# Performance work log

Hardware: AMD Instinct MI355X
Metric: run time of the kernel (lower is better)

The kernel has to match this reference:

```python
import jax, jax.numpy as jnp
import numpy as np

B, L, D_MODEL = 2, 2048, 1024
D_STATE, D_CONV, EXPAND, DT_RANK = 16, 4, 2, 64
D_INNER = EXPAND * D_MODEL


def setup_inputs() -> dict:
    key = jax.random.key(0)
    ks = jax.random.split(key, 12)
    s = 0.02
    A_log = jnp.log(jnp.broadcast_to(jnp.arange(1, D_STATE + 1, dtype=jnp.float32), (D_INNER, D_STATE)))
    return {
        "x": jax.random.normal(ks[0], (B, L, D_MODEL), jnp.float32),
        "W_in": jax.random.normal(ks[1], (2 * D_INNER, D_MODEL), jnp.float32) * s,
        "conv_w": jax.random.normal(ks[2], (D_INNER, 1, D_CONV), jnp.float32) * 0.2,
        "conv_b": jax.random.normal(ks[3], (D_INNER,), jnp.float32) * s,
        "W_xp": jax.random.normal(ks[4], (DT_RANK + 2 * D_STATE, D_INNER), jnp.float32) * s,
        "W_dt": jax.random.normal(ks[5], (D_INNER, DT_RANK), jnp.float32) * 0.1,
        "b_dt": jax.random.uniform(ks[6], (D_INNER,), jnp.float32, -4.6, -2.3),  # ~softplus^-1 of small dt
        "A_log": A_log,
        "D": jnp.ones((D_INNER,), jnp.float32),
        "W_out_ssm": jax.random.normal(ks[7], (D_MODEL, D_INNER), jnp.float32) * s,
        "W_out": jax.random.normal(ks[8], (D_MODEL, D_MODEL), jnp.float32) * s,
        "b_out": jnp.zeros((D_MODEL,), jnp.float32),
    }


def _mamba_block(x, W_in, conv_w, conv_b, W_xp, W_dt, b_dt, A_log, D, W_out_ssm, W_out, b_out):
    d_inner = conv_b.shape[0]
    d_state = A_log.shape[1]
    dt_rank = W_dt.shape[1]
    d_conv = conv_w.shape[-1]

    # in_proj -> x branch and gate z
    xz = x @ W_in.T                         # [B, L, 2*d_inner]
    xin, z = jnp.split(xz, 2, axis=-1)

    # causal depthwise conv over time
    xc = jnp.transpose(xin, (0, 2, 1))      # [B, d_inner, L]
    xc = jax.lax.conv_general_dilated(
        xc, conv_w, window_strides=(1,), padding=[(d_conv - 1, 0)],
        feature_group_count=d_inner)
    xc = jax.nn.silu(xc + conv_b[None, :, None])
    xs = jnp.transpose(xc, (0, 2, 1))       # [B, L, d_inner]

    # input-dependent dt, B, C
    x_dbl = xs @ W_xp.T                     # [B, L, dt_rank + 2*d_state]
    dt, Bm, Cm = jnp.split(x_dbl, [dt_rank, dt_rank + d_state], axis=-1)
    dt = jax.nn.softplus(dt @ W_dt.T + b_dt)  # [B, L, d_inner]

    A = -jnp.exp(A_log)                     # [d_inner, d_state]

    def step(h, inp):
        dt_t, B_t, C_t, x_t = inp           # [B,di] [B,ds] [B,ds] [B,di]
        dA = jnp.exp(dt_t[:, :, None] * A)                      # [B, di, ds]
        h = h * dA + (dt_t * x_t)[:, :, None] * B_t[:, None, :]  # [B, di, ds]
        y = jnp.einsum('bds,bs->bd', h, C_t)
        return h, y

    h0 = jnp.zeros((x.shape[0], d_inner, d_state), x.dtype)
    tm = lambda a: jnp.swapaxes(a, 0, 1)    # time-major
    _, ys = jax.lax.scan(step, h0, (tm(dt), tm(Bm), tm(Cm), tm(xs)))
    y = jnp.swapaxes(ys, 0, 1)              # [B, L, d_inner]

    y = y + xs * D
    y = y * jax.nn.silu(z)
    y = y @ W_out_ssm.T                     # mamba-internal out_proj -> d_model
    return y @ W_out.T + b_out              # wrapper out_proj


def reference(x, W_in, conv_w, conv_b, W_xp, W_dt, b_dt, A_log, D, W_out_ssm, W_out, b_out):
    return _mamba_block(x, W_in, conv_w, conv_b, W_xp, W_dt, b_dt, A_log, D, W_out_ssm, W_out, b_out)
```

## Files before the change

kernel.cpp:

```cpp
#include <hip/hip_runtime.h>
#include <hip/hip_bf16.h>
#include <cmath>
#include <cstdint>

typedef __bf16 bf16_t;
typedef bf16_t bf16x8 __attribute__((ext_vector_type(8)));
typedef bf16_t bf16x4 __attribute__((ext_vector_type(4)));
typedef float f32x4 __attribute__((ext_vector_type(4)));

#define BB 2
#define LL 2048
#define DMODEL 1024
#define DINNER 2048
#define DSTATE 16
#define NC 64
#define CHUNK 32
#define KSEG 256

#define EXP2F(x) __builtin_amdgcn_exp2f(x)

#define CVT_N0 1048576
#define CVT_N1 2097152
#define CVT_N2 2129920
#define CVT_N3 2392064
#define CVT_NB0 9344
#define CVT_NB1 10368
#define CVT_NBT 10880
__global__ __launch_bounds__(256) void k_cvt_all(
    const float* __restrict__ x, const float* __restrict__ Win,
    const float* __restrict__ Wdt, const float* __restrict__ Wo,
    const float* __restrict__ Wxp, const float* __restrict__ Wos,
    bf16_t* __restrict__ x_b, bf16_t* __restrict__ Win_b,
    bf16_t* __restrict__ Wdt_b, bf16_t* __restrict__ Wo_b,
    bf16_t* __restrict__ Wxp_b, bf16_t* __restrict__ WosT_b) {
    const int tid = threadIdx.x;
    if (blockIdx.x < CVT_NB0) {
        int i = blockIdx.x * 256 + tid;
        const float* src; bf16_t* dst; int j;
        if (i < CVT_N0)      { src = x;   dst = x_b;   j = i; }
        else if (i < CVT_N1) { src = Win; dst = Win_b; j = i - CVT_N0; }
        else if (i < CVT_N2) { src = Wdt; dst = Wdt_b; j = i - CVT_N1; }
        else                 { src = Wo;  dst = Wo_b;  j = i - CVT_N2; }
        float4 v = reinterpret_cast<const float4*>(src)[j];
        bf16x4 o;
        o[0] = (bf16_t)v.x; o[1] = (bf16_t)v.y; o[2] = (bf16_t)v.z; o[3] = (bf16_t)v.w;
        reinterpret_cast<bf16x4*>(dst)[j] = o;
    } else if (blockIdx.x < CVT_NB1) {
        int i = (blockIdx.x - CVT_NB0) * 256 + tid;
        int r = i >> 11, c = i & (DINNER - 1);
        float v = (r < 96) ? Wxp[r * DINNER + c] : 0.f;
        Wxp_b[i] = (bf16_t)v;
    } else {
        __shared__ float tile[64][65];
        const int bid = blockIdx.x - CVT_NB1;
        const int m0 = (bid & 15) * 64;
        const int d0 = (bid >> 4) * 64;
        const int dl = tid & 63;
        #pragma unroll 4
        for (int i = 0; i < 16; ++i) {
            const int mr = (tid >> 6) + i * 4;
            tile[dl][mr] = Wos[(size_t)(m0 + mr) * DINNER + d0 + dl];
        }
        __syncthreads();
        const int dr = tid >> 2;
        const int q  = tid & 3;
        bf16_t* op = WosT_b + (size_t)(d0 + dr) * DMODEL + m0 + q * 16;
        bf16x8 v0, v1;
        #pragma unroll
        for (int j = 0; j < 8; ++j) v0[j] = (bf16_t)tile[dr][q * 16 + j];
        #pragma unroll
        for (int j = 0; j < 8; ++j) v1[j] = (bf16_t)tile[dr][q * 16 + 8 + j];
        reinterpret_cast<bf16x8*>(op)[0] = v0;
        reinterpret_cast<bf16x8*>(op)[1] = v1;
    }
}

__device__ __forceinline__ void gload16(const void* g, void* l) {
    __builtin_amdgcn_global_load_lds(
        (const __attribute__((address_space(1))) void*)g,
        (__attribute__((address_space(3))) void*)l,
        16, 0, 0);
}

__global__ __launch_bounds__(512) void k_gemm256(
    const bf16_t* __restrict__ x_b, const bf16_t* __restrict__ Win_b,
    bf16_t* __restrict__ xin_b, bf16_t* __restrict__ zsT) {
    __shared__ bf16_t lds[65536];
    const int tid = threadIdx.x;
    const int wid = tid >> 6, lane = tid & 63;

    const int bid = (blockIdx.x & 7) * 32 + (blockIdx.x >> 3);
    const bf16_t* A; const bf16_t* Bt; int m0, n0, sub;
    if (bid < 128) {
        sub = 0; A = x_b; Bt = Win_b;
        m0 = (bid >> 3) * 256; n0 = (bid & 7) * 256;
    } else {
        sub = 1; A = Win_b + (size_t)DINNER * DMODEL; Bt = x_b;
        const int t2 = bid - 128;
        m0 = (t2 >> 4) * 256; n0 = (t2 & 15) * 256;
    }
    const int wr = wid >> 2, wc = wid & 3;
    f32x4 acc[8][4] = {};

    const int srow = tid >> 3;
    const int k8p = (tid & 7) ^ (srow & 7);
    const bf16_t* apA = A + (size_t)(m0 + srow) * 1024 + k8p * 8;
    const bf16_t* apB = Bt + (size_t)(n0 + srow) * 1024 + k8p * 8;

    auto stageA = [&](int slot, int kt) {
        char* b0 = (char*)lds + slot * 32768 + wid * 1024;
        const bf16_t* src = apA + kt * 64;
        gload16(src, b0);
        gload16(src + (size_t)64 * 1024, b0 + 8192);
        gload16(src + (size_t)128 * 1024, b0 + 16384);
        gload16(src + (size_t)192 * 1024, b0 + 24576);
    };
    auto stageB = [&](int slot, int kt) {
        char* b0 = (char*)lds + 65536 + slot * 32768 + wid * 1024;
        const bf16_t* src = apB + kt * 64;
        gload16(src, b0);
        gload16(src + (size_t)64 * 1024, b0 + 8192);
        gload16(src + (size_t)128 * 1024, b0 + 16384);
        gload16(src + (size_t)192 * 1024, b0 + 24576);
    };

    const int lm = lane & 15, lq = lane >> 4;

    const bf16_t* pA0[8]; const bf16_t* pA1[8];
    const bf16_t* pB0[4]; const bf16_t* pB1[4];
    #pragma unroll
    for (int i = 0; i < 8; ++i) {
        const int rr = lm + i * 16;
        const int e0 = wr * 8192 + rr * 64 + (lq ^ (rr & 7)) * 8;
        pA0[i] = lds + e0;
        pA1[i] = lds + (e0 ^ 32);
    }
    #pragma unroll
    for (int j = 0; j < 4; ++j) {
        const int rr = (wc & 1) * 64 + lm + j * 16;
        const int e0 = 32768 + (wc >> 1) * 8192 + rr * 64 + (lq ^ (rr & 7)) * 8;
        pB0[j] = lds + e0;
        pB1[j] = lds + (e0 ^ 32);
    }

    auto body = [&](int t, int s) {
        asm volatile("s_waitcnt vmcnt(0)" ::: "memory");
        __builtin_amdgcn_sched_barrier(0);
        __builtin_amdgcn_s_barrier();
        __builtin_amdgcn_sched_barrier(0);
        if (t + 1 < 16) {
            stageA(s ^ 1, t + 1);
            stageB(s ^ 1, t + 1);
        }
        {
            bf16x8 fa[8], fb[4];
            #pragma unroll
            for (int i = 0; i < 8; ++i) fa[i] = *(const bf16x8*)(pA0[i] + s * 16384);
            #pragma unroll
            for (int j = 0; j < 4; ++j) fb[j] = *(const bf16x8*)(pB0[j] + s * 16384);
            __builtin_amdgcn_s_setprio(1);
            #pragma unroll
            for (int i = 0; i < 8; ++i)
                #pragma unroll
                for (int j = 0; j < 4; ++j)
                    acc[i][j] = __builtin_amdgcn_mfma_f32_16x16x32_bf16(fa[i], fb[j], acc[i][j], 0, 0, 0);
            __builtin_amdgcn_s_setprio(0);
        }
        {
            bf16x8 fa[8], fb[4];
            #pragma unroll
            for (int i = 0; i < 8; ++i) fa[i] = *(const bf16x8*)(pA1[i] + s * 16384);
            #pragma unroll
            for (int j = 0; j < 4; ++j) fb[j] = *(const bf16x8*)(pB1[j] + s * 16384);
            __builtin_amdgcn_s_setprio(1);
            #pragma unroll
            for (int i = 0; i < 8; ++i)
                #pragma unroll
                for (int j = 0; j < 4; ++j)
                    acc[i][j] = __builtin_amdgcn_mfma_f32_16x16x32_bf16(fa[i], fb[j], acc[i][j], 0, 0, 0);
            __builtin_amdgcn_s_setprio(0);
        }
    };

    stageA(0, 0);
    stageB(0, 0);
    for (int tt = 0; tt < 8; ++tt) {
        body(2 * tt, 0);
        body(2 * tt + 1, 1);
    }

    const int row0 = m0 + wr * 128 + lq * 4;
    const int col0 = n0 + wc * 64 + lm;
    #pragma unroll
    for (int i = 0; i < 8; ++i) {
        #pragma unroll
        for (int j = 0; j < 4; ++j) {
            #pragma unroll
            for (int r = 0; r < 4; ++r) {
                const int row = row0 + i * 16 + r;
                const int c = col0 + j * 16;
                float v = acc[i][j][r];
                if (sub == 0) xin_b[(size_t)row * DINNER + c] = (bf16_t)v;
                else          zsT[(size_t)row * (BB * LL) + c] = (bf16_t)(v / (1.f + __expf(-v)));
            }
        }
    }
}

enum { EPI_BF16 = 0, EPI_BIAS = 1, EPI_SOFTPLUS_RB = 3, EPI_PARTK = 4 };

template <int EPI>
__global__ __launch_bounds__(512) void k_gemm_cd128(
    const bf16_t* __restrict__ A, const bf16_t* __restrict__ Bt,
    int N, int Ktiles, int lda, int ldb,
    float* __restrict__ C, bf16_t* __restrict__ Cb,
    const float* __restrict__ bias) {
    __shared__ bf16_t lds[32768];
    const int tid = threadIdx.x;
    const int wid = tid >> 6, lane = tid & 63;
    const int bx = (blockIdx.x & 7) * ((int)gridDim.x >> 3) + (blockIdx.x >> 3);
    const int ntile = N >> 7;
    const int m0 = (bx / ntile) << 7;
    const int n0 = (bx % ntile) << 7;
    const int wr = wid >> 2, wc = wid & 3;
    f32x4 acc[4][2] = {};

    const int srow = tid >> 3;
    const int k8p = (tid & 7) ^ (srow & 7);
    const bf16_t* apA = A + (size_t)(m0 + srow) * lda + k8p * 8;
    const bf16_t* apB = Bt + (size_t)(n0 + srow) * ldb + k8p * 8;

    auto stageA = [&](int slot, int kt) {
        char* b0 = (char*)lds + slot * 16384 + wid * 1024;
        const bf16_t* src = apA + kt * 64;
        gload16(src, b0);
        gload16(src + (size_t)64 * lda, b0 + 8192);
    };
    auto stageB = [&](int slot, int kt) {
        char* b0 = (char*)lds + 32768 + slot * 16384 + wid * 1024;
        const bf16_t* src = apB + kt * 64;
        gload16(src, b0);
        gload16(src + (size_t)64 * ldb, b0 + 8192);
    };

    const int lm = lane & 15, lq = lane >> 4;

    const bf16_t* pA0[4]; const bf16_t* pA1[4];
    const bf16_t* pB0[2]; const bf16_t* pB1[2];
    #pragma unroll
    for (int i = 0; i < 4; ++i) {
        const int rr = lm + i * 16;
        const int e0 = wr * 4096 + rr * 64 + (lq ^ (rr & 7)) * 8;
        pA0[i] = lds + e0;
        pA1[i] = lds + (e0 ^ 32);
    }
    #pragma unroll
    for (int j = 0; j < 2; ++j) {
        const int rr = wc * 32 + lm + j * 16;
        const int e0 = 16384 + rr * 64 + (lq ^ (rr & 7)) * 8;
        pB0[j] = lds + e0;
        pB1[j] = lds + (e0 ^ 32);
    }

    auto body = [&](int t, int s) {
        asm volatile("s_waitcnt vmcnt(0)" ::: "memory");
        __builtin_amdgcn_sched_barrier(0);
        __builtin_amdgcn_s_barrier();
        __builtin_amdgcn_sched_barrier(0);
        if (t + 1 < Ktiles) {
            stageA(s ^ 1, t + 1);
            stageB(s ^ 1, t + 1);
        }
        {
            bf16x8 fa[4], fb[2];
            #pragma unroll
            for (int i = 0; i < 4; ++i) fa[i] = *(const bf16x8*)(pA0[i] + s * 8192);
            #pragma unroll
            for (int j = 0; j < 2; ++j) fb[j] = *(const bf16x8*)(pB0[j] + s * 8192);
            __builtin_amdgcn_s_setprio(1);
            #pragma unroll
            for (int i = 0; i < 4; ++i)
                #pragma unroll
                for (int j = 0; j < 2; ++j)
                    acc[i][j] = __builtin_amdgcn_mfma_f32_16x16x32_bf16(fa[i], fb[j], acc[i][j], 0, 0, 0);
            __builtin_amdgcn_s_setprio(0);
        }
        {
            bf16x8 fa[4], fb[2];
            #pragma unroll
            for (int i = 0; i < 4; ++i) fa[i] = *(const bf16x8*)(pA1[i] + s * 8192);
            #pragma unroll
            for (int j = 0; j < 2; ++j) fb[j] = *(const bf16x8*)(pB1[j] + s * 8192);
            __builtin_amdgcn_s_setprio(1);
            #pragma unroll
            for (int i = 0; i < 4; ++i)
                #pragma unroll
                for (int j = 0; j < 2; ++j)
                    acc[i][j] = __builtin_amdgcn_mfma_f32_16x16x32_bf16(fa[i], fb[j], acc[i][j], 0, 0, 0);
            __builtin_amdgcn_s_setprio(0);
        }
    };

    stageA(0, 0);
    stageB(0, 0);
    for (int tt = 0; tt < (Ktiles >> 1); ++tt) {
        body(2 * tt, 0);
        body(2 * tt + 1, 1);
    }

    const int row0 = m0 + wr * 64 + lq * 4;
    const int col0 = n0 + wc * 32 + lm;
    #pragma unroll
    for (int i = 0; i < 4; ++i) {
        #pragma unroll
        for (int j = 0; j < 2; ++j) {
            #pragma unroll
            for (int r = 0; r < 4; ++r) {
                const int row = row0 + i * 16 + r;
                const int c = col0 + j * 16;
                float v = acc[i][j][r];
                if (EPI == EPI_BF16) Cb[(size_t)row * N + c] = (bf16_t)v;
                else                 C[(size_t)row * N + c] = v + bias[c];
            }
        }
    }
}

template <int EPI>
__global__ __launch_bounds__(512) void k_gemm_bt(
    const bf16_t* __restrict__ A, const bf16_t* __restrict__ Bt,
    int M, int N, int Kloop, int lda, int ldb,
    float* __restrict__ C, bf16_t* __restrict__ Cb,
    const float* __restrict__ bias,
    float* __restrict__ o_part) {
    __shared__ bf16_t sA[2][128 * 32];
    __shared__ bf16_t sB[2][128 * 32];
    const int tid = threadIdx.x;
    const int wid = tid >> 6, lane = tid & 63;
    const int bx = (blockIdx.x & 7) * ((int)gridDim.x >> 3) + (blockIdx.x >> 3);
    int m0, n0, k0 = 0, seg = 0;
    if (EPI == EPI_PARTK) {
        m0 = (bx & 31) << 7;
        n0 = 0;
        seg = bx >> 5;
        k0 = seg * KSEG;
    } else {
        const int ntile = N >> 7;
        m0 = (bx / ntile) << 7;
        n0 = (bx % ntile) << 7;
    }
    const int wr = wid >> 2, wc = wid & 3;
    f32x4 acc[4][2] = {};

    const bf16_t* ap = A + (size_t)(m0 + (tid >> 2)) * lda + (tid & 3) * 8 + k0;
    const bf16_t* bp = Bt + (size_t)(n0 + (tid >> 2)) * ldb + (tid & 3) * 8 + k0;
    const int lm = lane & 15, lk = (lane >> 4) * 8;

    auto stage = [&](int buf, int kt) {
        char* dA = (char*)sA[buf] + wid * 1024;
        char* dB = (char*)sB[buf] + wid * 1024;
        gload16(ap + kt, dA);
        gload16(bp + kt, dB);
    };

    stage(0, 0);
    __syncthreads();
    int cur = 0;
    for (int kt = 0; kt < Kloop; kt += 32) {
        if (kt + 32 < Kloop) stage(cur ^ 1, kt + 32);
        const bf16_t* rA = sA[cur] + (wr * 64 + lm) * 32 + lk;
        const bf16_t* rB = sB[cur] + (wc * 32 + lm) * 32 + lk;
        bf16x8 fa[4], fb[2];
        #pragma unroll
        for (int i = 0; i < 4; ++i) fa[i] = *(const bf16x8*)(rA + i * 16 * 32);
        #pragma unroll
        for (int j = 0; j < 2; ++j) fb[j] = *(const bf16x8*)(rB + j * 16 * 32);
        __builtin_amdgcn_s_setprio(1);
        #pragma unroll
        for (int i = 0; i < 4; ++i)
            #pragma unroll
            for (int j = 0; j < 2; ++j)
                acc[i][j] = __builtin_amdgcn_mfma_f32_16x16x32_bf16(fa[i], fb[j], acc[i][j], 0, 0, 0);
        __builtin_amdgcn_s_setprio(0);
        __syncthreads();
        cur ^= 1;
    }

    const int row0 = m0 + wr * 64 + (lane >> 4) * 4;
    const int col0 = n0 + wc * 32 + lm;
    float* Cp = (EPI == EPI_PARTK)
        ? o_part + (size_t)seg * ((size_t)4096 * 128)
        : C;
    #pragma unroll
    for (int i = 0; i < 4; ++i) {
        #pragma unroll
        for (int j = 0; j < 2; ++j) {
            #pragma unroll
            for (int r = 0; r < 4; ++r) {
                int row = row0 + i * 16 + r;
                int c = col0 + j * 16;
                float v = acc[i][j][r];
                if (EPI == EPI_SOFTPLUS_RB) {
                    float xv = v + bias[row];
                    float sp = fmaxf(xv, 0.f) + log1pf(__expf(-fabsf(xv)));
                    Cb[(size_t)row * N + c] = (bf16_t)sp;
                } else {
                    Cp[(size_t)row * 128 + c] = v;
                }
            }
        }
    }
}

__global__ __launch_bounds__(256) void k_split_reduce(
    const float* __restrict__ part, bf16_t* __restrict__ dtr,
    float* __restrict__ Bmf, float* __restrict__ Cmf) {
    int idx = blockIdx.x * 256 + threadIdx.x;
    int row = idx >> 7, c = idx & 127;
    float s = 0.f;
    #pragma unroll
    for (int g = 0; g < 8; ++g) s += part[(size_t)g * (4096 * 128) + idx];
    if (c < 64) dtr[(size_t)row * 64 + c] = (bf16_t)s;
    else if (c < 80) Bmf[(size_t)row * 16 + (c - 64)] = s;
    else if (c < 96) Cmf[(size_t)row * 16 + (c - 80)] = s;
}

__global__ __launch_bounds__(256) void k_conv(
    const bf16_t* __restrict__ xin, const float* __restrict__ cw,
    const float* __restrict__ cb, bf16_t* __restrict__ xs_b,
    bf16_t* __restrict__ xsT) {
    __shared__ float tile[64][65];
    const int tid = threadIdx.x;
    const int d0  = (blockIdx.x & 31) * 64;
    const int bl0 = (blockIdx.x >> 5) * 64;
    const int dl = tid & 63;
    const int d  = d0 + dl;
    const float w0 = cw[d * 4], w1 = cw[d * 4 + 1], w2 = cw[d * 4 + 2], w3 = cw[d * 4 + 3];
    const float bias = cb[d];
    const int l0 = bl0 & (LL - 1);
    #pragma unroll 4
    for (int i = 0; i < 16; ++i) {
        const int blr = (tid >> 6) + i * 4;
        const int bl = bl0 + blr;
        const int l  = l0 + blr;
        const bf16_t* rp = xin + (size_t)bl * DINNER + d;
        float acc = fmaf(w3, (float)rp[0], bias);
        if (l >= 1) acc = fmaf(w2, (float)rp[-(int)DINNER], acc);
        if (l >= 2) acc = fmaf(w1, (float)rp[-2 * (int)DINNER], acc);
        if (l >= 3) acc = fmaf(w0, (float)rp[-3 * (int)DINNER], acc);
        float sv = acc / (1.f + __expf(-acc));
        xs_b[(size_t)bl * DINNER + d] = (bf16_t)sv;
        tile[dl][blr] = sv;
    }
    __syncthreads();
    const int dr = tid >> 2;
    const int q  = tid & 3;
    bf16_t* op = xsT + (size_t)(d0 + dr) * (BB * LL) + bl0 + q * 16;
    bf16x8 v0, v1;
    #pragma unroll
    for (int j = 0; j < 8; ++j) v0[j] = (bf16_t)tile[dr][q * 16 + j];
    #pragma unroll
    for (int j = 0; j < 8; ++j) v1[j] = (bf16_t)tile[dr][q * 16 + 8 + j];
    reinterpret_cast<bf16x8*>(op)[0] = v0;
    reinterpret_cast<bf16x8*>(op)[1] = v1;
}


__global__ __launch_bounds__(256) void k_scan_p1(
    const bf16_t* __restrict__ dtT, const bf16_t* __restrict__ xsT,
    const float* __restrict__ Bm, const float* __restrict__ A_log,
    bf16_t* __restrict__ alpha, bf16_t* __restrict__ beta) {
    __shared__ float sB[CHUNK * 16];
    const int db = blockIdx.x & 7;
    const int ck = (blockIdx.x >> 3) & (NC - 1);
    const int b  = blockIdx.x >> 9;
    const int tid = threadIdx.x;
    const int d  = db * 256 + tid;
    const int t0 = ck * CHUNK;

    const float* Bsrc = Bm + ((size_t)b * LL + t0) * 16;
    sB[tid] = Bsrc[tid];
    sB[tid + 256] = Bsrc[tid + 256];

    f32x4 a2[4];
    #pragma unroll
    for (int q = 0; q < 4; ++q) {
        f32x4 av = reinterpret_cast<const f32x4*>(A_log + d * 16)[q];
        #pragma unroll
        for (int j = 0; j < 4; ++j) a2[q][j] = -__expf(av[j]) * 1.44269504f;
    }
    const bf16x8* dtp = reinterpret_cast<const bf16x8*>(dtT + (size_t)d * (BB * LL) + b * LL + t0);
    const bf16x8* xsp = reinterpret_cast<const bf16x8*>(xsT + (size_t)d * (BB * LL) + b * LL + t0);

    bf16x8 dtl[4], xsl[4];
    #pragma unroll
    for (int q = 0; q < 4; ++q) dtl[q] = dtp[q];
    #pragma unroll
    for (int q = 0; q < 4; ++q) xsl[q] = xsp[q];

    __syncthreads();

    float al[16], be[16];
    #pragma unroll
    for (int s = 0; s < 16; ++s) { al[s] = 1.f; be[s] = 0.f; }

    #pragma unroll
    for (int t = 0; t < CHUNK; ++t) {
        float dtv = (float)dtl[t >> 3][t & 7];
        float xv  = (float)xsl[t >> 3][t & 7];
        float dtx = dtv * xv;
        #pragma unroll
        for (int q = 0; q < 4; ++q) {
            f32x4 Bq = *reinterpret_cast<const f32x4*>(sB + t * 16 + q * 4);
            #pragma unroll
            for (int j = 0; j < 4; ++j) {
                const int s = q * 4 + j;
                float dA = EXP2F(dtv * a2[q][j]);
                al[s] *= dA;
                be[s] = fmaf(be[s], dA, dtx * Bq[j]);
            }
        }
    }
    bf16_t* ap = alpha + ((size_t)(b * NC + ck)) * (DINNER * 16) + (size_t)d * 16;
    bf16_t* bp = beta  + ((size_t)(b * NC + ck)) * (DINNER * 16) + (size_t)d * 16;
    bf16x8 av0, av1, bv0, bv1;
    #pragma unroll
    for (int j = 0; j < 8; ++j) {
        av0[j] = (bf16_t)al[j];     av1[j] = (bf16_t)al[8 + j];
        bv0[j] = (bf16_t)be[j];     bv1[j] = (bf16_t)be[8 + j];
    }
    reinterpret_cast<bf16x8*>(ap)[0] = av0;
    reinterpret_cast<bf16x8*>(ap)[1] = av1;
    reinterpret_cast<bf16x8*>(bp)[0] = bv0;
    reinterpret_cast<bf16x8*>(bp)[1] = bv1;
}

__global__ __launch_bounds__(256) void k_scan_p2(
    const bf16_t* __restrict__ alpha, const bf16_t* __restrict__ beta,
    bf16_t* __restrict__ H) {
    const int gid = blockIdx.x * 256 + threadIdx.x;
    const int b = gid >> 15, r = gid & 32767;
    float h = 0.f;
    #pragma unroll 8
    for (int ck = 0; ck < NC; ++ck) {
        const size_t i = ((size_t)(b * NC + ck)) * 32768 + r;
        H[i] = (bf16_t)h;
        h = fmaf((float)alpha[i], h, (float)beta[i]);
    }
}

__global__ __launch_bounds__(256) void k_scan_p3(
    const bf16_t* __restrict__ dtT, const bf16_t* __restrict__ xsT,
    const float* __restrict__ Bm, const float* __restrict__ Cm,
    const bf16_t* __restrict__ zsT, const float* __restrict__ A_log,
    const float* __restrict__ Dp, const bf16_t* __restrict__ H,
    bf16_t* __restrict__ y) {
    __shared__ float sB[CHUNK * 16];
    __shared__ float sC[CHUNK * 16];
    const int db = blockIdx.x & 7;
    const int ck = (blockIdx.x >> 3) & (NC - 1);
    const int b  = blockIdx.x >> 9;
    const int tid = threadIdx.x;
    const int d  = db * 256 + tid;
    const int t0 = ck * CHUNK;

    const float* Bsrc = Bm + ((size_t)b * LL + t0) * 16;
    const float* Csrc = Cm + ((size_t)b * LL + t0) * 16;
    sB[tid] = Bsrc[tid];
    sB[tid + 256] = Bsrc[tid + 256];
    sC[tid] = Csrc[tid];
    sC[tid + 256] = Csrc[tid + 256];

    f32x4 a2[4];
    #pragma unroll
    for (int q = 0; q < 4; ++q) {
        f32x4 av = reinterpret_cast<const f32x4*>(A_log + d * 16)[q];
        #pragma unroll
        for (int j = 0; j < 4; ++j) a2[q][j] = -__expf(av[j]) * 1.44269504f;
    }
    const float Dd = Dp[d];
    const bf16x8* dtp = reinterpret_cast<const bf16x8*>(dtT + (size_t)d * (BB * LL) + b * LL + t0);
    const bf16x8* xsp = reinterpret_cast<const bf16x8*>(xsT + (size_t)d * (BB * LL) + b * LL + t0);
    const bf16x8* zp  = reinterpret_cast<const bf16x8*>(zsT + (size_t)d * (BB * LL) + b * LL + t0);
    bf16_t* yp = y + ((size_t)b * LL + t0) * DINNER + d;

    bf16x8 dtl[4], xsl[4], zsl[4];
    #pragma unroll
    for (int q = 0; q < 4; ++q) dtl[q] = dtp[q];
    #pragma unroll
    for (int q = 0; q < 4; ++q) xsl[q] = xsp[q];
    #pragma unroll
    for (int q = 0; q < 4; ++q) zsl[q] = zp[q];

    float h[16];
    {
        const bf16x8* hp = reinterpret_cast<const bf16x8*>(H + ((size_t)(b * NC + ck)) * 32768 + (size_t)d * 16);
        bf16x8 h0 = hp[0], h1 = hp[1];
        #pragma unroll
        for (int j = 0; j < 8; ++j) { h[j] = (float)h0[j]; h[8 + j] = (float)h1[j]; }
    }

    __syncthreads();

    #pragma unroll
    for (int t = 0; t < CHUNK; ++t) {
        float dtv = (float)dtl[t >> 3][t & 7];
        float xv  = (float)xsl[t >> 3][t & 7];
        float zv  = (float)zsl[t >> 3][t & 7];
        float dtx = dtv * xv;
        float yacc = 0.f;
        #pragma unroll
        for (int q = 0; q < 4; ++q) {
            f32x4 Bq = *reinterpret_cast<const f32x4*>(sB + t * 16 + q * 4);
            f32x4 Cq = *reinterpret_cast<const f32x4*>(sC + t * 16 + q * 4);
            #pragma unroll
            for (int j = 0; j < 4; ++j) {
                const int s = q * 4 + j;
                float dA = EXP2F(dtv * a2[q][j]);
                h[s] = fmaf(h[s], dA, dtx * Bq[j]);
                yacc = fmaf(h[s], Cq[j], yacc);
            }
        }
        float yv = (yacc + xv * Dd) * zv;
        yp[(size_t)t * DINNER] = (bf16_t)yv;
    }
}

extern "C" void kernel_launch(void* const* d_in, const int* in_sizes, int n_in,
                              void* d_out, int out_size, void* d_ws, size_t ws_size,
                              hipStream_t stream) {
    const float* x      = (const float*)d_in[0];
    const float* W_in   = (const float*)d_in[1];
    const float* conv_w = (const float*)d_in[2];
    const float* conv_b = (const float*)d_in[3];
    const float* W_xp   = (const float*)d_in[4];
    const float* W_dt   = (const float*)d_in[5];
    const float* b_dt   = (const float*)d_in[6];
    const float* A_log  = (const float*)d_in[7];
    const float* Dvec   = (const float*)d_in[8];
    const float* W_os   = (const float*)d_in[9];
    const float* W_o    = (const float*)d_in[10];
    const float* b_o    = (const float*)d_in[11];
    float* out = (float*)d_out;

    char* base = (char*)d_ws;
    size_t off = 0;
    auto alloc = [&](size_t bytes) -> char* {
        char* p = base + off;
        off += (bytes + 255) & ~(size_t)255;
        return p;
    };
    const int MR = BB * LL;
    bf16_t* x_b   = (bf16_t*)alloc((size_t)MR * DMODEL * 2);
    bf16_t* Win_b = (bf16_t*)alloc((size_t)4096 * 1024 * 2);
    bf16_t* xin_b = (bf16_t*)alloc((size_t)MR * DINNER * 2);
    bf16_t* xs_b  = (bf16_t*)alloc((size_t)MR * DINNER * 2);
    bf16_t* zsT   = (bf16_t*)alloc((size_t)DINNER * MR * 2);
    bf16_t* xsT   = (bf16_t*)alloc((size_t)DINNER * MR * 2);
    bf16_t* dtT_b = (bf16_t*)alloc((size_t)DINNER * MR * 2);
    float*  Hbuf  = (float*)alloc((size_t)BB * NC * DINNER * 16 * 4);
    bf16_t* y_b   = (bf16_t*)alloc((size_t)MR * DINNER * 2);
    bf16_t* dtr_b = (bf16_t*)alloc((size_t)MR * 64 * 2);
    float*  Bmf   = (float*)alloc((size_t)MR * 16 * 4);
    float*  Cmf   = (float*)alloc((size_t)MR * 16 * 4);
    bf16_t* Wxp_b = (bf16_t*)alloc((size_t)128 * DINNER * 2);
    bf16_t* Wdt_b = (bf16_t*)alloc((size_t)DINNER * 64 * 2);
    bf16_t* WosT_b= (bf16_t*)alloc((size_t)DINNER * DMODEL * 2);
    bf16_t* Wo_b  = (bf16_t*)alloc((size_t)DMODEL * DMODEL * 2);
    bf16_t* Wc_b  = (bf16_t*)alloc((size_t)DMODEL * DINNER * 2);

    bf16_t* alphab = (bf16_t*)xin_b;
    bf16_t* betab  = (bf16_t*)x_b;
    float*  partk  = Hbuf;
    bf16_t* Hb     = (bf16_t*)Hbuf;

    k_cvt_all<<<CVT_NBT, 256, 0, stream>>>(
        x, W_in, W_dt, W_o, W_xp, W_os,
        x_b, Win_b, Wdt_b, Wo_b, Wxp_b, WosT_b);

    k_gemm_cd128<EPI_BF16><<<(DMODEL / 128) * (DINNER / 128), 512, 0, stream>>>(
        Wo_b, WosT_b, DINNER, 16, DMODEL, DMODEL, nullptr, Wc_b, nullptr);
    k_gemm256<<<256, 512, 0, stream>>>(x_b, Win_b, xin_b, zsT);
    k_conv<<<(MR / 64) * (DINNER / 64), 256, 0, stream>>>(xin_b, conv_w, conv_b, xs_b, xsT);
    k_gemm_bt<EPI_PARTK><<<8 * 32, 512, 0, stream>>>(
        xs_b, Wxp_b, MR, 128, KSEG, DINNER, DINNER,
        nullptr, nullptr, nullptr, partk);
    k_split_reduce<<<(MR * 128) / 256, 256, 0, stream>>>(partk, dtr_b, Bmf, Cmf);
    k_gemm_bt<EPI_SOFTPLUS_RB><<<(DINNER / 128) * (MR / 128), 512, 0, stream>>>(
        Wdt_b, dtr_b, DINNER, MR, 64, 64, 64,
        nullptr, dtT_b, b_dt, nullptr);
    k_scan_p1<<<BB * NC * (DINNER / 256), 256, 0, stream>>>(dtT_b, xsT, Bmf, A_log, alphab, betab);
    k_scan_p2<<<(BB * DINNER * DSTATE) / 256, 256, 0, stream>>>(alphab, betab, Hb);
    k_scan_p3<<<BB * NC * (DINNER / 256), 256, 0, stream>>>(dtT_b, xsT, Bmf, Cmf, zsT, A_log, Dvec, Hb, y_b);
    k_gemm_cd128<EPI_BIAS><<<(MR / 128) * (DMODEL / 128), 512, 0, stream>>>(
        y_b, Wc_b, DMODEL, 32, DINNER, DINNER, out, nullptr, b_o);
}
```

Baseline: 221.0 us.

## Use 4-stage K=32 LDS pipeline with partial vmcnt waits in in_proj GEMM

The in_proj GEMM tile loop moves from a double-buffered K=64 stage to a four-slot ring of K=32 stages, prefetching three tiles ahead. The wait before each step now checks a partial vmcnt rather than draining all outstanding loads, so global loads overlap with several MFMA steps. The LDS swizzle and fragment addressing are reworked for the narrower 32-element rows. The trade-off is more barriers per K (32 steps instead of 16) and less MFMA work between barriers.

New measurement: 225.4 us. Within noise of the previous version (+2.0%).

```diff
diff --git a/kernel.cpp b/kernel.cpp
--- a/kernel.cpp
+++ b/kernel.cpp
@@ -102,91 +102,72 @@
     const int wr = wid >> 2, wc = wid & 3;
     f32x4 acc[8][4] = {};
 
-    const int srow = tid >> 3;
-    const int k8p = (tid & 7) ^ (srow & 7);
+    const int srow = tid >> 2;
+    const int k8p = (tid & 3) ^ ((tid >> 3) & 3);
     const bf16_t* apA = A + (size_t)(m0 + srow) * 1024 + k8p * 8;
     const bf16_t* apB = Bt + (size_t)(n0 + srow) * 1024 + k8p * 8;
 
     auto stageA = [&](int slot, int kt) {
-        char* b0 = (char*)lds + slot * 32768 + wid * 1024;
-        const bf16_t* src = apA + kt * 64;
+        char* b0 = (char*)lds + slot * 16384 + wid * 1024;
+        const bf16_t* src = apA + kt * 32;
         gload16(src, b0);
-        gload16(src + (size_t)64 * 1024, b0 + 8192);
-        gload16(src + (size_t)128 * 1024, b0 + 16384);
-        gload16(src + (size_t)192 * 1024, b0 + 24576);
+        gload16(src + (size_t)128 * 1024, b0 + 8192);
     };
     auto stageB = [&](int slot, int kt) {
-        char* b0 = (char*)lds + 65536 + slot * 32768 + wid * 1024;
-        const bf16_t* src = apB + kt * 64;
+        char* b0 = (char*)lds + 65536 + slot * 16384 + wid * 1024;
+        const bf16_t* src = apB + kt * 32;
         gload16(src, b0);
-        gload16(src + (size_t)64 * 1024, b0 + 8192);
-        gload16(src + (size_t)128 * 1024, b0 + 16384);
-        gload16(src + (size_t)192 * 1024, b0 + 24576);
+        gload16(src + (size_t)128 * 1024, b0 + 8192);
     };
 
     const int lm = lane & 15, lq = lane >> 4;
-
-    const bf16_t* pA0[8]; const bf16_t* pA1[8];
-    const bf16_t* pB0[4]; const bf16_t* pB1[4];
+    const int csw = (lq ^ ((lm >> 1) & 3)) * 8;
+
+    const bf16_t* pA[8]; const bf16_t* pB[4];
     #pragma unroll
     for (int i = 0; i < 8; ++i) {
-        const int rr = lm + i * 16;
-        const int e0 = wr * 8192 + rr * 64 + (lq ^ (rr & 7)) * 8;
-        pA0[i] = lds + e0;
-        pA1[i] = lds + (e0 ^ 32);
+        const int rr = wr * 128 + i * 16 + lm;
+        pA[i] = lds + rr * 32 + csw;
     }
     #pragma unroll
     for (int j = 0; j < 4; ++j) {
-        const int rr = (wc & 1) * 64 + lm + j * 16;
-        const int e0 = 32768 + (wc >> 1) * 8192 + rr * 64 + (lq ^ (rr & 7)) * 8;
-        pB0[j] = lds + e0;
-        pB1[j] = lds + (e0 ^ 32);
+        const int rr = wc * 64 + j * 16 + lm;
+        pB[j] = lds + 32768 + rr * 32 + csw;
     }
 
     auto body = [&](int t, int s) {
-        asm volatile("s_waitcnt vmcnt(0)" ::: "memory");
+        if (t < 30)       asm volatile("s_waitcnt vmcnt(8)" ::: "memory");
+        else if (t == 30) asm volatile("s_waitcnt vmcnt(4)" ::: "memory");
+        else              asm volatile("s_waitcnt vmcnt(0)" ::: "memory");
         __builtin_amdgcn_sched_barrier(0);
         __builtin_amdgcn_s_barrier();
         __builtin_amdgcn_sched_barrier(0);
-        if (t + 1 < 16) {
-            stageA(s ^ 1, t + 1);
-            stageB(s ^ 1, t + 1);
-        }
-        {
-            bf16x8 fa[8], fb[4];
-            #pragma unroll
-            for (int i = 0; i < 8; ++i) fa[i] = *(const bf16x8*)(pA0[i] + s * 16384);
-            #pragma unroll
-            for (int j = 0; j < 4; ++j) fb[j] = *(const bf16x8*)(pB0[j] + s * 16384);
-            __builtin_amdgcn_s_setprio(1);
-            #pragma unroll
-            for (int i = 0; i < 8; ++i)
-                #pragma unroll
-                for (int j = 0; j < 4; ++j)
-                    acc[i][j] = __builtin_amdgcn_mfma_f32_16x16x32_bf16(fa[i], fb[j], acc[i][j], 0, 0, 0);
-            __builtin_amdgcn_s_setprio(0);
-        }
-        {
-            bf16x8 fa[8], fb[4];
-            #pragma unroll
-            for (int i = 0; i < 8; ++i) fa[i] = *(const bf16x8*)(pA1[i] + s * 16384);
-            #pragma unroll
-            for (int j = 0; j < 4; ++j) fb[j] = *(const bf16x8*)(pB1[j] + s * 16384);
-            __builtin_amdgcn_s_setprio(1);
-            #pragma unroll
-            for (int i = 0; i < 8; ++i)
-                #pragma unroll
-                for (int j = 0; j < 4; ++j)
-                    acc[i][j] = __builtin_amdgcn_mfma_f32_16x16x32_bf16(fa[i], fb[j], acc[i][j], 0, 0, 0);
-            __builtin_amdgcn_s_setprio(0);
-        }
-    };
-
-    stageA(0, 0);
-    stageB(0, 0);
-    for (int tt = 0; tt < 8; ++tt) {
-        body(2 * tt, 0);
-        body(2 * tt + 1, 1);
+        if (t + 3 < 32) {
+            stageA((s + 3) & 3, t + 3);
+            stageB((s + 3) & 3, t + 3);
+        }
+        bf16x8 fa[8], fb[4];
+        #pragma unroll
+        for (int i = 0; i < 8; ++i) fa[i] = *(const bf16x8*)(pA[i] + s * 8192);
+        #pragma unroll
+        for (int j = 0; j < 4; ++j) fb[j] = *(const bf16x8*)(pB[j] + s * 8192);
+        __builtin_amdgcn_s_setprio(1);
+        #pragma unroll
+        for (int i = 0; i < 8; ++i)
+            #pragma unroll
+            for (int j = 0; j < 4; ++j)
+                acc[i][j] = __builtin_amdgcn_mfma_f32_16x16x32_bf16(fa[i], fb[j], acc[i][j], 0, 0, 0);
+        __builtin_amdgcn_s_setprio(0);
+    };
+
+    stageA(0, 0); stageB(0, 0);
+    stageA(1, 1); stageB(1, 1);
+    stageA(2, 2); stageB(2, 2);
+    for (int q = 0; q < 8; ++q) {
+        body(4 * q, 0);
+        body(4 * q + 1, 1);
+        body(4 * q + 2, 2);
+        body(4 * q + 3, 3);
     }
 
     const int row0 = m0 + wr * 128 + lq * 4;
```
